# Kernel optimization log

Hardware: AMD Instinct MI355X
Metric: run time of the kernel (lower is better)

## Reference

```python
import jax, jax.numpy as jnp
import numpy as np

NUM_LEVELS = 16
BASE_RES = 16
MAX_RES = 2048
F_PER_LEVEL = 2
MAX_TABLE = 524288  # 2**19
N_POINTS = 1048576
# geometric resolution schedule, identical to the torch module
RESOLUTIONS = [int(BASE_RES * (MAX_RES / BASE_RES) ** (l / (NUM_LEVELS - 1))) for l in range(NUM_LEVELS)]
TABLE_SIZES = [min(r ** 3, MAX_TABLE) for r in RESOLUTIONS]


def setup_inputs() -> dict:
    key = jax.random.key(0)
    k0, k1, k2, k3 = jax.random.split(key, 4)
    coords = jax.random.uniform(k0, (N_POINTS, 3), minval=-1.0, maxval=1.0, dtype=jnp.float32)
    # hash tables init U(-1e-4, 1e-4); all padded to MAX_TABLE rows (levels with
    # smaller dense tables simply never index past TABLE_SIZES[l])
    tables = jax.random.uniform(k1, (NUM_LEVELS, MAX_TABLE, F_PER_LEVEL), minval=-1e-4, maxval=1e-4, dtype=jnp.float32)
    d_in = NUM_LEVELS * F_PER_LEVEL  # 32
    W1 = jax.random.normal(k2, (d_in, 128), dtype=jnp.float32) * (2.0 / (d_in + 128)) ** 0.5
    b1 = jnp.zeros((128,), dtype=jnp.float32)
    W2 = jax.random.normal(k3, (128, 64), dtype=jnp.float32) * (2.0 / (128 + 64)) ** 0.5
    b2 = jnp.zeros((64,), dtype=jnp.float32)
    return {"coords": coords, "tables": tables, "W1": W1, "b1": b1, "W2": W2, "b2": b2}


def _hash_gather(coords, tables):
    # coords: [N, 3] in [-1, 1] -> normalized to [0, 1]
    c = (coords + 1.0) * 0.5
    feats = []
    for l in range(NUM_LEVELS):
        R = RESOLUTIONS[l]
        T = TABLE_SIZES[l]
        d = jnp.clip(jnp.floor(c * R).astype(jnp.int32), 0, R - 1).astype(jnp.uint32)  # [N, 3]
        # (x*R^2 + y*R + z) % T in uint32. Wraparound mod 2^32 only occurs at the
        # finest levels where T = 2^19 divides 2^32, so the result stays exact.
        idx = (d[:, 0] * jnp.uint32(R * R) + d[:, 1] * jnp.uint32(R) + d[:, 2]) % jnp.uint32(T)
        feats.append(tables[l][idx.astype(jnp.int32)])  # [N, F_PER_LEVEL]
    return jnp.concatenate(feats, axis=-1)  # [N, 32], level-major


def reference(coords, tables, W1, b1, W2, b2):
    x = _hash_gather(coords, tables)              # [N, 32]
    h = jax.nn.relu(x @ W1 + b1)                  # [N, 128]
    return h @ W2 + b2                            # [N, 64]
```

## Files before the change

### kernel.cpp

```cpp
#include <hip/hip_runtime.h>
#include <stdint.h>


typedef __attribute__((ext_vector_type(8))) __bf16 bf16x8;
typedef __attribute__((ext_vector_type(4))) float  f32x4;
typedef __attribute__((ext_vector_type(2))) float  f32x2;

#define NPTS   1048576
#define NTILES 65536

__device__ const unsigned kRES[16] = {16u,22u,30u,42u,58u,80u,111u,153u,
                                      212u,294u,406u,561u,776u,1072u,1482u,2048u};

__device__ __forceinline__ unsigned pack_bf16(float x, float y) {
  __bf16 a = (__bf16)x, b = (__bf16)y;
  unsigned short ua, ub;
  __builtin_memcpy(&ua, &a, 2);
  __builtin_memcpy(&ub, &b, 2);
  return (unsigned)ua | ((unsigned)ub << 16);
}

__global__ void prep_kernel(const float* __restrict__ W1, const float* __restrict__ W2,
                            short* __restrict__ w1p, short* __restrict__ w2p) {
  int tid = blockIdx.x * blockDim.x + threadIdx.x;
  int l = tid & 63;
  int g = l >> 4;
  int c = l & 15;
  if (tid < 512) {
    int t = tid >> 6;
    bf16x8 v;
#pragma unroll
    for (int j = 0; j < 8; ++j)
      v[j] = (__bf16)W1[(8*g + j)*128 + 16*t + c];
    *(bf16x8*)(w1p + (size_t)(t*64 + l)*8) = v;
  } else if (tid < 1536) {
    int e = (tid - 512) >> 6;
    int mt = e >> 2, ks = e & 3;
    bf16x8 v;
#pragma unroll
    for (int j = 0; j < 8; ++j)
      v[j] = (__bf16)W2[(32*ks + 16*(j>>2) + 4*g + (j&3))*64 + 16*mt + c];
    *(bf16x8*)(w2p + (size_t)(e*64 + l)*8) = v;
  }
}

__global__ __launch_bounds__(256) void gather_kernel(
    const float* __restrict__ coords, const float* __restrict__ tables,
    unsigned* __restrict__ xw)
{
  const int xcd = blockIdx.x & 7;
  const int j   = blockIdx.x >> 3;
  int lv, chunk;
  if (j < 1408) {
    int ghi = xcd * 1408 + j;
    lv = 5 + (ghi >> 10);
    chunk = ghi & 1023;
  } else {
    int gei = xcd * 640 + (j - 1408);
    lv = gei >> 10;
    chunk = gei & 1023;
  }

  const unsigned R = kRES[lv];
  const float fR = (float)R;
  const unsigned RR = R * R;
  const unsigned Rm1 = R - 1u;
  const unsigned M = (lv >= 6) ? 0x7FFFFu : 0xFFFFFFFFu;
  const float* tb = tables + ((size_t)lv << 20);
  unsigned* xp = xw + ((size_t)lv << 20);

  int p0 = chunk * 1024 + threadIdx.x;
#pragma unroll
  for (int i = 0; i < 4; ++i) {
    int p = p0 + (i << 8);
    float u0 = (coords[3*p+0] + 1.0f) * 0.5f;
    float u1 = (coords[3*p+1] + 1.0f) * 0.5f;
    float u2 = (coords[3*p+2] + 1.0f) * 0.5f;
    unsigned d0 = (unsigned)(int)(u0 * fR); if (d0 > Rm1) d0 = Rm1;
    unsigned d1 = (unsigned)(int)(u1 * fR); if (d1 > Rm1) d1 = Rm1;
    unsigned d2 = (unsigned)(int)(u2 * fR); if (d2 > Rm1) d2 = Rm1;
    unsigned idx = (d0*RR + d1*R + d2) & M;
    f32x2 f = *(const f32x2*)(tb + (size_t)idx*2u);
    xp[p] = pack_bf16(f.x, f.y);
  }
}

__global__ __launch_bounds__(256, 4) void mlp_kernel(
    const unsigned* __restrict__ xw,
    const float* __restrict__ b1, const float* __restrict__ b2,
    const short* __restrict__ w1p, const short* __restrict__ w2p,
    float* __restrict__ out)
{
  const int l = threadIdx.x & 63;
  const int g = l >> 4;
  const int c = l & 15;
  const int w = threadIdx.x >> 6;

  __shared__ float obuf[4][16][68];

  bf16x8 w1f[8];
#pragma unroll
  for (int t = 0; t < 8; ++t)
    w1f[t] = *(const bf16x8*)(w1p + (size_t)(t*64 + l)*8);

  const int base = blockIdx.x * 4 + w;

  unsigned gx[4][4];
#pragma unroll
  for (int it = 0; it < 4; ++it) {
    int p = (base + it*16384)*16 + c;
#pragma unroll
    for (int q = 0; q < 4; ++q)
      gx[it][q] = xw[((size_t)(4*g + q) << 20) + p];
  }

#pragma unroll
  for (int it = 0; it < 4; ++it) {
    union { bf16x8 v; unsigned u[4]; } X;
#pragma unroll
    for (int q = 0; q < 4; ++q) X.u[q] = gx[it][q];
    bf16x8 xf = X.v;

    f32x4 h[8];
#pragma unroll
    for (int t = 0; t < 8; ++t) {
      h[t] = *(const f32x4*)(b1 + 16*t + 4*g);
      h[t] = __builtin_amdgcn_mfma_f32_16x16x32_bf16(w1f[t], xf, h[t], 0, 0, 0);
    }

    f32x4 o[4];
#pragma unroll
    for (int mt = 0; mt < 4; ++mt)
      o[mt] = *(const f32x4*)(b2 + 16*mt + 4*g);
#pragma unroll
    for (int ks = 0; ks < 4; ++ks) {
      bf16x8 bp;
#pragma unroll
      for (int j = 0; j < 8; ++j) {
        float v = h[2*ks + (j>>2)][j & 3];
        v = fmaxf(v, 0.0f);
        bp[j] = (__bf16)v;
      }
#pragma unroll
      for (int mt = 0; mt < 4; ++mt) {
        bf16x8 w2f = *(const bf16x8*)(w2p + (size_t)((mt*4 + ks)*64 + l)*8);
        o[mt] = __builtin_amdgcn_mfma_f32_16x16x32_bf16(w2f, bp, o[mt], 0, 0, 0);
      }
    }

    float (*ob)[68] = obuf[w];
#pragma unroll
    for (int mt = 0; mt < 4; ++mt)
      *(f32x4*)&ob[c][16*mt + 4*g] = o[mt];
    asm volatile("s_waitcnt lgkmcnt(0)" ::: "memory");
    f32x4 v[4];
#pragma unroll
    for (int s = 0; s < 4; ++s)
      v[s] = *(const f32x4*)&ob[4*s + g][4*c];
    asm volatile("" ::: "memory");
    float* op = out + (size_t)(base + it*16384) * 1024;
#pragma unroll
    for (int s = 0; s < 4; ++s)
      *(f32x4*)(op + (4*s + g)*64 + 4*c) = v[s];

    if (it < 3) asm volatile("s_waitcnt lgkmcnt(0)" ::: "memory");
  }
}

__global__ __launch_bounds__(256, 3) void hashgrid_mlp_kernel(
    const float* __restrict__ coords, const float* __restrict__ tables,
    const float* __restrict__ b1, const float* __restrict__ b2,
    const short* __restrict__ w1p, const short* __restrict__ w2p,
    float* __restrict__ out, int stride)
{
  const int l = threadIdx.x & 63;
  const int g = l >> 4;
  const int c = l & 15;

  unsigned Rq[4], RRq[4], Mq[4]; float fRq[4];
#pragma unroll
  for (int q = 0; q < 4; ++q) {
    int lv = 4*g + q;
    unsigned R = kRES[lv];
    Rq[q] = R; RRq[q] = R*R; fRq[q] = (float)R;
    Mq[q] = (lv >= 6) ? 0x7FFFFu : 0xFFFFFFFFu;
  }
  const float* tb = tables + ((size_t)g << 22);

  bf16x8 w1f[8];
#pragma unroll
  for (int t = 0; t < 8; ++t)
    w1f[t] = *(const bf16x8*)(w1p + (size_t)(t*64 + l)*8);

  f32x2 gx[4];
  auto prefetch = [&](int tile) {
    int p = tile*16 + c;
    float u0 = (coords[3*p+0] + 1.0f) * 0.5f;
    float u1 = (coords[3*p+1] + 1.0f) * 0.5f;
    float u2 = (coords[3*p+2] + 1.0f) * 0.5f;
#pragma unroll
    for (int q = 0; q < 4; ++q) {
      unsigned Rm1 = Rq[q] - 1u;
      unsigned d0 = (unsigned)(int)(u0 * fRq[q]); if (d0 > Rm1) d0 = Rm1;
      unsigned d1 = (unsigned)(int)(u1 * fRq[q]); if (d1 > Rm1) d1 = Rm1;
      unsigned d2 = (unsigned)(int)(u2 * fRq[q]); if (d2 > Rm1) d2 = Rm1;
      unsigned idx = (d0*RRq[q] + d1*Rq[q] + d2) & Mq[q];
      gx[q] = *(const f32x2*)(tb + ((size_t)q << 20) + (size_t)idx*2u);
    }
  };

  int tile = blockIdx.x * 4 + (threadIdx.x >> 6);
  prefetch(tile);
  while (true) {
    bf16x8 xf;
#pragma unroll
    for (int q = 0; q < 4; ++q) {
      xf[2*q]   = (__bf16)gx[q].x;
      xf[2*q+1] = (__bf16)gx[q].y;
    }
    int cur = tile;
    tile += stride;
    if (tile < NTILES) prefetch(tile);

    f32x4 h[8];
#pragma unroll
    for (int t = 0; t < 8; ++t) {
      h[t] = *(const f32x4*)(b1 + 16*t + 4*g);
      h[t] = __builtin_amdgcn_mfma_f32_16x16x32_bf16(w1f[t], xf, h[t], 0, 0, 0);
    }

    f32x4 o[4];
#pragma unroll
    for (int mt = 0; mt < 4; ++mt)
      o[mt] = *(const f32x4*)(b2 + 16*mt + 4*g);
#pragma unroll
    for (int ks = 0; ks < 4; ++ks) {
      bf16x8 bp;
#pragma unroll
      for (int j = 0; j < 8; ++j) {
        float v = h[2*ks + (j>>2)][j & 3];
        v = fmaxf(v, 0.0f);
        bp[j] = (__bf16)v;
      }
#pragma unroll
      for (int mt = 0; mt < 4; ++mt) {
        bf16x8 w2f = *(const bf16x8*)(w2p + (size_t)((mt*4 + ks)*64 + l)*8);
        o[mt] = __builtin_amdgcn_mfma_f32_16x16x32_bf16(w2f, bp, o[mt], 0, 0, 0);
      }
    }

    float* op = out + (size_t)(cur*16 + c)*64 + 4*g;
#pragma unroll
    for (int mt = 0; mt < 4; ++mt)
      *(f32x4*)(op + 16*mt) = o[mt];

    if (tile >= NTILES) break;
  }
}

extern "C" void kernel_launch(void* const* d_in, const int* in_sizes, int n_in,
                              void* d_out, int out_size, void* d_ws, size_t ws_size,
                              hipStream_t stream) {
  const float* coords = (const float*)d_in[0];
  const float* tables = (const float*)d_in[1];
  const float* W1     = (const float*)d_in[2];
  const float* b1     = (const float*)d_in[3];
  const float* W2     = (const float*)d_in[4];
  const float* b2     = (const float*)d_in[5];
  float* out = (float*)d_out;

  short* w1p = (short*)d_ws;
  short* w2p = w1p + 4096;
  prep_kernel<<<6, 256, 0, stream>>>(W1, W2, w1p, w2p);

  const size_t need = 32*1024 + (size_t)NPTS * 16 * 4;
  if (ws_size >= need) {
    unsigned* xw = (unsigned*)((char*)d_ws + 32*1024);
    gather_kernel<<<16384, 256, 0, stream>>>(coords, tables, xw);
    mlp_kernel<<<4096, 256, 0, stream>>>(xw, b1, b2, w1p, w2p, out);
  } else {
    const int blocks = 2048;
    hashgrid_mlp_kernel<<<blocks, 256, 0, stream>>>(coords, tables, b1, b2,
                                                    w1p, w2p, out, blocks*4);
  }
}
```

Before: 194.1 us.

## Pre-convert hash tables to packed bf16 before the gather pass

Adds a pre-pass, merged with the weight-prep kernel, that converts every hash table entry from two fp32 values to one packed bf16 word in workspace. The gather kernel then reads 4-byte entries instead of 8-byte ones, halving the bytes per random access and the table's cache footprint. The cost is an extra full streaming pass over the 64 MB table each call (read 64 MB, write 32 MB) plus larger workspace needs. It also raises the workspace threshold for the two-pass path, so a smaller workspace falls back to the fused kernel.

```diff
diff --git a/kernel.cpp b/kernel.cpp
--- a/kernel.cpp
+++ b/kernel.cpp
@@ -20,9 +20,22 @@
   return (unsigned)ua | ((unsigned)ub << 16);
 }
 
-__global__ void prep_kernel(const float* __restrict__ W1, const float* __restrict__ W2,
-                            short* __restrict__ w1p, short* __restrict__ w2p) {
-  int tid = blockIdx.x * blockDim.x + threadIdx.x;
+__global__ __launch_bounds__(256) void tconv_prep_kernel(
+    const float* __restrict__ tables,
+    const float* __restrict__ W1, const float* __restrict__ W2,
+    unsigned* __restrict__ tb2, short* __restrict__ w1p, short* __restrict__ w2p)
+{
+  if (blockIdx.x < 8192) {
+    int e0 = (blockIdx.x * 256 + threadIdx.x) * 4;
+#pragma unroll
+    for (int i = 0; i < 4; ++i) {
+      int e = e0 + i;
+      f32x2 f = *(const f32x2*)(tables + (size_t)e * 2);
+      tb2[e] = pack_bf16(f.x, f.y);
+    }
+    return;
+  }
+  int tid = (blockIdx.x - 8192) * 256 + threadIdx.x;
   int l = tid & 63;
   int g = l >> 4;
   int c = l & 15;
@@ -45,7 +58,7 @@
 }
 
 __global__ __launch_bounds__(256) void gather_kernel(
-    const float* __restrict__ coords, const float* __restrict__ tables,
+    const float* __restrict__ coords, const unsigned* __restrict__ tb2,
     unsigned* __restrict__ xw)
 {
   const int xcd = blockIdx.x & 7;
@@ -66,7 +79,7 @@
   const unsigned RR = R * R;
   const unsigned Rm1 = R - 1u;
   const unsigned M = (lv >= 6) ? 0x7FFFFu : 0xFFFFFFFFu;
-  const float* tb = tables + ((size_t)lv << 20);
+  const unsigned* tb = tb2 + ((size_t)lv << 19);
   unsigned* xp = xw + ((size_t)lv << 20);
 
   int p0 = chunk * 1024 + threadIdx.x;
@@ -80,8 +93,7 @@
     unsigned d1 = (unsigned)(int)(u1 * fR); if (d1 > Rm1) d1 = Rm1;
     unsigned d2 = (unsigned)(int)(u2 * fR); if (d2 > Rm1) d2 = Rm1;
     unsigned idx = (d0*RR + d1*R + d2) & M;
-    f32x2 f = *(const f32x2*)(tb + (size_t)idx*2u);
-    xp[p] = pack_bf16(f.x, f.y);
+    xp[p] = tb[idx];
   }
 }
 
@@ -167,6 +179,30 @@
   }
 }
 
+__global__ void prep_kernel(const float* __restrict__ W1, const float* __restrict__ W2,
+                            short* __restrict__ w1p, short* __restrict__ w2p) {
+  int tid = blockIdx.x * blockDim.x + threadIdx.x;
+  int l = tid & 63;
+  int g = l >> 4;
+  int c = l & 15;
+  if (tid < 512) {
+    int t = tid >> 6;
+    bf16x8 v;
+#pragma unroll
+    for (int j = 0; j < 8; ++j)
+      v[j] = (__bf16)W1[(8*g + j)*128 + 16*t + c];
+    *(bf16x8*)(w1p + (size_t)(t*64 + l)*8) = v;
+  } else if (tid < 1536) {
+    int e = (tid - 512) >> 6;
+    int mt = e >> 2, ks = e & 3;
+    bf16x8 v;
+#pragma unroll
+    for (int j = 0; j < 8; ++j)
+      v[j] = (__bf16)W2[(32*ks + 16*(j>>2) + 4*g + (j&3))*64 + 16*mt + c];
+    *(bf16x8*)(w2p + (size_t)(e*64 + l)*8) = v;
+  }
+}
+
 __global__ __launch_bounds__(256, 3) void hashgrid_mlp_kernel(
     const float* __restrict__ coords, const float* __restrict__ tables,
     const float* __restrict__ b1, const float* __restrict__ b2,
@@ -271,14 +307,20 @@
 
   short* w1p = (short*)d_ws;
   short* w2p = w1p + 4096;
-  prep_kernel<<<6, 256, 0, stream>>>(W1, W2, w1p, w2p);
-
-  const size_t need = 32*1024 + (size_t)NPTS * 16 * 4;
+
+  const size_t XW_OFF  = 32*1024;
+  const size_t XW_SZ   = (size_t)NPTS * 16 * 4;
+  const size_t TB2_SZ  = (size_t)16 * 524288 * 4;
+  const size_t need = XW_OFF + XW_SZ + TB2_SZ;
+
   if (ws_size >= need) {
-    unsigned* xw = (unsigned*)((char*)d_ws + 32*1024);
-    gather_kernel<<<16384, 256, 0, stream>>>(coords, tables, xw);
+    unsigned* xw  = (unsigned*)((char*)d_ws + XW_OFF);
+    unsigned* tb2 = (unsigned*)((char*)d_ws + XW_OFF + XW_SZ);
+    tconv_prep_kernel<<<8198, 256, 0, stream>>>(tables, W1, W2, tb2, w1p, w2p);
+    gather_kernel<<<16384, 256, 0, stream>>>(coords, tb2, xw);
     mlp_kernel<<<4096, 256, 0, stream>>>(xw, b1, b2, w1p, w2p, out);
   } else {
+    prep_kernel<<<6, 256, 0, stream>>>(W1, W2, w1p, w2p);
     const int blocks = 2048;
     hashgrid_mlp_kernel<<<blocks, 256, 0, stream>>>(coords, tables, b1, b2,
                                                     w1p, w2p, out, blocks*4);
```

After: 188.3 us. -3.0%, faster.
